# Optimization experiments

Hardware: AMD Instinct MI355X
Metric: run time of the kernel (lower is better)

## Reference

```python
import jax, jax.numpy as jnp
import numpy as np

GROUPS = 8
EPS = 1e-3  # Keras GroupNormalization default epsilon


def group_norm(x, gamma, beta):
    b, h, w, c = x.shape
    xr = x.reshape(b, h, w, GROUPS, c // GROUPS)
    mean = jnp.mean(xr, axis=(1, 2, 4), keepdims=True)
    var = jnp.var(xr, axis=(1, 2, 4), keepdims=True)
    xn = ((xr - mean) * jax.lax.rsqrt(var + EPS)).reshape(b, h, w, c)
    return xn * gamma + beta


def setup_inputs() -> dict:
    key = jax.random.key(0)
    ks = jax.random.split(key, 6)
    B, H, W, C = 4, 64, 64, 256
    std = C ** -0.5
    return {
        "x": jax.random.normal(ks[0], (B, H, W, C), dtype=jnp.float32),
        "gamma": jnp.ones((C,), jnp.float32),
        "beta": jnp.zeros((C,), jnp.float32),
        "wq": jax.random.normal(ks[1], (C, C), jnp.float32) * std,
        "bq": jnp.zeros((C,), jnp.float32),
        "wk": jax.random.normal(ks[2], (C, C), jnp.float32) * std,
        "bk": jnp.zeros((C,), jnp.float32),
        "wv": jax.random.normal(ks[3], (C, C), jnp.float32) * std,
        "bv": jnp.zeros((C,), jnp.float32),
        "wp": jax.random.normal(ks[4], (C, C), jnp.float32) * std,
        "bp": jnp.zeros((C,), jnp.float32),
    }


def reference(x, gamma, beta, wq, bq, wk, bk, wv, bv, wp, bp):
    b, h, w, c = x.shape
    scale = jnp.asarray(c, x.dtype) ** -0.5
    xn = group_norm(x, gamma, beta)
    # 1x1 convs are per-pixel dense layers
    q = (xn @ wq + bq).reshape(b, h * w, c)
    k = (xn @ wk + bk).reshape(b, h * w, c)
    v = (xn @ wv + bv).reshape(b, h * w, c)
    scores = jnp.einsum('bic,bjc->bij', q, k) * scale  # [b, N, N]
    attn = jax.nn.softmax(scores, axis=-1)
    out = jnp.einsum('bij,bjc->bic', attn, v).reshape(b, h, w, c)
    return x + (out @ wp + bp)
```

## Files before the change

kernel.cpp:

```cpp
#include <hip/hip_runtime.h>

#define N_TOK 4096
#define C_DIM 256
#define BATCH 4
#define M_ROWS (BATCH * N_TOK)
#define GN_CNT 131072.0f
#define JSPLIT 4

typedef __attribute__((ext_vector_type(4))) float f32x4;
typedef __attribute__((ext_vector_type(16))) float f32x16;
typedef __attribute__((ext_vector_type(8))) short s16x8;
typedef __attribute__((ext_vector_type(4))) unsigned short u16x4;
typedef __attribute__((ext_vector_type(4))) unsigned int u32x4;

static __device__ __forceinline__ unsigned short f2bf(float f) {
  unsigned int u = __builtin_bit_cast(unsigned int, f);
  u += 0x7fff + ((u >> 16) & 1);
  return (unsigned short)(u >> 16);
}
static __device__ __forceinline__ float bf2f(unsigned short h) {
  unsigned int u = ((unsigned int)h) << 16;
  return __builtin_bit_cast(float, u);
}

static __device__ __forceinline__ void gload_lds16(const void* g, void* l) {
  __builtin_amdgcn_global_load_lds(
      (__attribute__((address_space(1))) void*)(unsigned long long)(const char*)g,
      (__attribute__((address_space(3))) void*)l, 16, 0, 0);
}

__global__ __launch_bounds__(256) void prep(const float* __restrict__ x,
                                            const float* __restrict__ wq,
                                            const float* __restrict__ wk,
                                            const float* __restrict__ wv,
                                            const float* __restrict__ wp,
                                            float* __restrict__ partials,
                                            unsigned short* __restrict__ wT) {
  int tid = threadIdx.x;
  if (blockIdx.x < 512) {
    int bg = blockIdx.x >> 4, chunk = blockIdx.x & 15;
    int b = bg >> 3, g = bg & 7;
    const f32x4* x4 = (const f32x4*)x;
    float s1 = 0.f, s2 = 0.f;
#pragma unroll
    for (int it = 0; it < 8; ++it) {
      int idx = it * 256 + tid;
      int nl = idx >> 3, cq = idx & 7;
      f32x4 v = x4[(b * N_TOK + chunk * 256 + nl) * 64 + g * 8 + cq];
      s1 += v[0] + v[1] + v[2] + v[3];
      s2 += v[0] * v[0] + v[1] * v[1] + v[2] * v[2] + v[3] * v[3];
    }
    for (int m = 1; m < 64; m <<= 1) {
      s1 += __shfl_xor(s1, m, 64);
      s2 += __shfl_xor(s2, m, 64);
    }
    __shared__ float r1[4], r2[4];
    int wave = tid >> 6, lane = tid & 63;
    if (lane == 0) { r1[wave] = s1; r2[wave] = s2; }
    __syncthreads();
    if (tid == 0) {
      int slot = (bg * 16 + chunk) * 2;
      partials[slot]     = r1[0] + r1[1] + r1[2] + r1[3];
      partials[slot + 1] = r2[0] + r2[1] + r2[2] + r2[3];
    }
  } else {
    int rem = blockIdx.x - 512;
    int z = rem >> 6, t = rem & 63;
    int k0 = (t >> 3) * 32, n0 = (t & 7) * 32;
    const float* const srcs[4] = {wq, wk, wv, wp};
    const float* w = srcs[z];
    unsigned short* o = wT + z * 65536;
    __shared__ float tt[32][33];
    int tx = tid & 31, ty = tid >> 5;
#pragma unroll
    for (int ky = 0; ky < 32; ky += 8)
      tt[ty + ky][tx] = w[(k0 + ty + ky) * C_DIM + n0 + tx];
    __syncthreads();
#pragma unroll
    for (int ky = 0; ky < 32; ky += 8)
      o[(n0 + ty + ky) * C_DIM + k0 + tx] = f2bf(tt[tx][ty + ky]);
  }
}

__global__ __launch_bounds__(256, 2) void qkv_gemm(const float* __restrict__ x,
                                                   const unsigned short* __restrict__ wT,
                                                   const float* __restrict__ partials,
                                                   const float* __restrict__ gamma,
                                                   const float* __restrict__ beta,
                                                   const float* __restrict__ bq,
                                                   const float* __restrict__ bk,
                                                   const float* __restrict__ bv,
                                                   unsigned short* __restrict__ qo,
                                                   unsigned short* __restrict__ ko,
                                                   unsigned short* __restrict__ vo) {
  int tid = threadIdx.x;
  int wave = tid >> 6, lane = tid & 63, n32 = lane & 31, half = lane >> 5;
  int row0 = blockIdx.x * 128 + wave * 32;
  int c0 = blockIdx.y * 128;
  int row = row0 + n32;
  int batch = blockIdx.x >> 5;
  __shared__ __align__(16) unsigned short Wt[32768];
  __shared__ float mean_s[8], rstd_s[8];

#pragma unroll
  for (int ii = 0; ii < 32; ++ii) {
    int u = ii * 256 + tid;
    int n = u >> 5, ku = u & 31;
    gload_lds16(wT + (size_t)(c0 + n) * C_DIM + ((ku ^ (n & 7)) * 8), Wt + u * 8);
  }
  if (tid < 8) {
    const float* p = partials + (batch * 8 + tid) * 32;
    float s1 = 0.f, s2 = 0.f;
#pragma unroll
    for (int c = 0; c < 16; ++c) { s1 += p[2 * c]; s2 += p[2 * c + 1]; }
    float inv = 1.f / GN_CNT;
    float m = s1 * inv, v = s2 * inv - m * m;
    mean_s[tid] = m;
    rstd_s[tid] = rsqrtf(v + 1e-3f);
  }
  __syncthreads();

  float mean[8], rstd[8];
#pragma unroll
  for (int g = 0; g < 8; ++g) { mean[g] = mean_s[g]; rstd[g] = rstd_s[g]; }
  s16x8 af[16];
#pragma unroll
  for (int ks = 0; ks < 16; ++ks) {
    int cb = ks * 16 + half * 8;
    const f32x4* xp = (const f32x4*)(x + (size_t)row * C_DIM + cb);
    f32x4 v0 = xp[0], v1 = xp[1];
    const f32x4* g4 = (const f32x4*)(gamma + cb);
    const f32x4* b4 = (const f32x4*)(beta + cb);
    f32x4 ga0 = g4[0], ga1 = g4[1], be0 = b4[0], be1 = b4[1];
    int g = (2 * ks + half) >> 2;
    float m = mean[g], rs = rstd[g];
    s16x8 o;
#pragma unroll
    for (int j = 0; j < 4; ++j) {
      o[j]     = (short)f2bf((v0[j] - m) * rs * ga0[j] + be0[j]);
      o[4 + j] = (short)f2bf((v1[j] - m) * rs * ga1[j] + be1[j]);
    }
    af[ks] = o;
  }

  for (int w = 0; w < 3; ++w) {
    if (w > 0) {
      __syncthreads();
#pragma unroll
      for (int ii = 0; ii < 32; ++ii) {
        int u = ii * 256 + tid;
        int n = u >> 5, ku = u & 31;
        gload_lds16(wT + (size_t)w * 65536 + (size_t)(c0 + n) * C_DIM + ((ku ^ (n & 7)) * 8),
                    Wt + u * 8);
      }
      __syncthreads();
    }
    const float* bias = (w == 0) ? bq : (w == 1) ? bk : bv;
    unsigned short* outp = (w == 0) ? qo : (w == 1) ? ko : vo;
    float scale = (w == 0) ? 0.0625f : 1.f;
#pragma unroll
    for (int ct = 0; ct < 4; ++ct) {
      int nl = ct * 32 + n32;
      f32x16 acc = (f32x16)(bias[c0 + nl]);
#pragma unroll
      for (int ks = 0; ks < 16; ++ks) {
        s16x8 wf = *(const s16x8*)(Wt + nl * C_DIM + (((2 * ks + half) ^ (nl & 7)) * 8));
        acc = __builtin_amdgcn_mfma_f32_32x32x16_bf16(af[ks], wf, acc, 0, 0, 0);
      }
#pragma unroll
      for (int r = 0; r < 16; ++r) {
        int rr = (r & 3) + 8 * (r >> 2) + 4 * half;
        outp[(size_t)(row0 + rr) * C_DIM + c0 + nl] = f2bf(acc[r] * scale);
      }
    }
  }
}

__global__ __launch_bounds__(256) void vtrans(const unsigned short* __restrict__ v,
                                              unsigned short* __restrict__ vT) {
  __shared__ unsigned short t[32][33];
  int n0 = blockIdx.x * 32, c0 = blockIdx.y * 32, b = blockIdx.z;
  int tx = threadIdx.x, ty = threadIdx.y;
#pragma unroll
  for (int ky = 0; ky < 32; ky += 8)
    t[ty + ky][tx] = v[(b * N_TOK + n0 + ty + ky) * C_DIM + c0 + tx];
  __syncthreads();
#pragma unroll
  for (int ky = 0; ky < 32; ky += 8)
    vT[(b * C_DIM + c0 + ty + ky) * N_TOK + n0 + tx] = t[tx][ty + ky];
}

static __device__ __forceinline__ void stage_K(unsigned short* dst,
                                               const unsigned short* kb,
                                               int jbase, int tid) {
#pragma unroll
  for (int ii = 0; ii < 4; ++ii) {
    int u = ii * 256 + tid;
    int ksu = u >> 6, tok = (u >> 1) & 31, hf = u & 1;
    gload_lds16(kb + (size_t)(jbase + tok) * C_DIM + ksu * 16 + hf * 8, dst + u * 8);
  }
}
static __device__ __forceinline__ void stage_V(unsigned short* dst,
                                               const unsigned short* vb,
                                               int jbase, int tid) {
#pragma unroll
  for (int ii = 0; ii < 4; ++ii)
    gload_lds16(vb + (size_t)tid * N_TOK + jbase + ii * 8, dst + (ii * 256 + tid) * 8);
}

static __device__ __forceinline__ f32x16 qk_compute(const unsigned short* KT,
                                                    const s16x8* qf,
                                                    int n32, int half) {
  f32x16 sc = (f32x16)(0.f);
#pragma unroll
  for (int ks = 0; ks < 16; ++ks) {
    s16x8 kf = *(const s16x8*)(KT + ks * 512 + (n32 * 2 + half) * 8);
    sc = __builtin_amdgcn_mfma_f32_32x32x16_bf16(kf, qf[ks], sc, 0, 0, 0);
  }
  return sc;
}

__global__ __launch_bounds__(256, 2) void attn_part(const unsigned short* __restrict__ q,
                                                    const unsigned short* __restrict__ k,
                                                    const unsigned short* __restrict__ vT,
                                                    unsigned short* __restrict__ op0,
                                                    unsigned short* __restrict__ op1,
                                                    unsigned short* __restrict__ op2,
                                                    unsigned short* __restrict__ op3,
                                                    float* __restrict__ lbuf) {
  int tid = threadIdx.x;
  int wave = tid >> 6, lane = tid & 63;
  int n32 = lane & 31, half = lane >> 5;
  int i = blockIdx.x;
  int batch = (i >> 1) & 3;
  int slot = ((i >> 3) << 1) | (i & 1);
  int qb = slot & 31, chunk = slot >> 5;
  int qrow0 = batch * N_TOK + qb * 128 + wave * 32;
  const unsigned short* kb = k + (size_t)batch * N_TOK * C_DIM;
  const unsigned short* vb = vT + (size_t)batch * C_DIM * N_TOK;
  unsigned short* op = (chunk == 0) ? op0 : (chunk == 1) ? op1 : (chunk == 2) ? op2 : op3;

  __shared__ __align__(16) unsigned short K_lds[2][8192];
  __shared__ __align__(16) unsigned short V_lds[3][8192];

  int jbase0 = chunk * 1024;
  stage_K(K_lds[0], kb, jbase0, tid);
  stage_V(V_lds[0], vb, jbase0, tid);

  const unsigned short* qp = q + (size_t)(qrow0 + n32) * C_DIM;
  s16x8 qf[16];
#pragma unroll
  for (int ks = 0; ks < 16; ++ks)
    qf[ks] = *(const s16x8*)(qp + ks * 16 + half * 8);

  f32x16 Oa[8];
#pragma unroll
  for (int ct = 0; ct < 8; ++ct) Oa[ct] = (f32x16)(0.f);
  float ls = 0.f;

  __syncthreads();

  stage_K(K_lds[1], kb, jbase0 + 32, tid);
  stage_V(V_lds[1], vb, jbase0 + 32, tid);

  s16x8 pf0p, pf1p;
  {
    f32x16 sc = qk_compute(K_lds[0], qf, n32, half);
    unsigned D[8], E[8];
#pragma unroll
    for (int t = 0; t < 8; ++t) {
      float pa = exp2f(fmaf(sc[2 * t],     1.44269504f, -11.54156032f));
      float pb = exp2f(fmaf(sc[2 * t + 1], 1.44269504f, -11.54156032f));
      ls += pa + pb;
      D[t] = (__builtin_bit_cast(unsigned, pa) >> 16) |
             (__builtin_bit_cast(unsigned, pb) & 0xFFFF0000u);
      E[t] = __shfl_xor(D[t], 32);
    }
    u32x4 w0 = {half ? E[2] : D[0], half ? E[3] : D[1],
                half ? D[2] : E[0], half ? D[3] : E[1]};
    u32x4 w1 = {half ? E[6] : D[4], half ? E[7] : D[5],
                half ? D[6] : E[4], half ? D[7] : E[5]};
    pf0p = __builtin_bit_cast(s16x8, w0);
    pf1p = __builtin_bit_cast(s16x8, w1);
  }

  int vr_i = 0, vw_i = 2;
  for (int jt = 1; jt < 32; ++jt) {
    __syncthreads();
    if (jt < 31) {
      int jb2 = jbase0 + (jt + 1) * 32;
      stage_K(K_lds[(jt + 1) & 1], kb, jb2, tid);
      stage_V(V_lds[vw_i], vb, jb2, tid);
    }
    __builtin_amdgcn_s_setprio(1);
    f32x16 sc = qk_compute(K_lds[jt & 1], qf, n32, half);

    const unsigned short* VR = V_lds[vr_i];
    unsigned D[8], E[8];
#pragma unroll
    for (int t = 0; t < 8; ++t) {
      float pa = exp2f(fmaf(sc[2 * t],     1.44269504f, -11.54156032f));
      float pb = exp2f(fmaf(sc[2 * t + 1], 1.44269504f, -11.54156032f));
      ls += pa + pb;
      D[t] = (__builtin_bit_cast(unsigned, pa) >> 16) |
             (__builtin_bit_cast(unsigned, pb) & 0xFFFF0000u);
      E[t] = __shfl_xor(D[t], 32);
      int ch = t * 32 + n32;
      s16x8 vf0 = *(const s16x8*)(VR + (half * 256 + ch) * 8);
      s16x8 vf1 = *(const s16x8*)(VR + ((2 + half) * 256 + ch) * 8);
      Oa[t] = __builtin_amdgcn_mfma_f32_32x32x16_bf16(pf0p, vf0, Oa[t], 0, 0, 0);
      Oa[t] = __builtin_amdgcn_mfma_f32_32x32x16_bf16(pf1p, vf1, Oa[t], 0, 0, 0);
    }
    __builtin_amdgcn_s_setprio(0);

    u32x4 w0 = {half ? E[2] : D[0], half ? E[3] : D[1],
                half ? D[2] : E[0], half ? D[3] : E[1]};
    u32x4 w1 = {half ? E[6] : D[4], half ? E[7] : D[5],
                half ? D[6] : E[4], half ? D[7] : E[5]};
    pf0p = __builtin_bit_cast(s16x8, w0);
    pf1p = __builtin_bit_cast(s16x8, w1);
    vr_i = (vr_i == 2) ? 0 : vr_i + 1;
    vw_i = (vw_i == 2) ? 0 : vw_i + 1;
  }

  {
    const unsigned short* VR = V_lds[vr_i];
#pragma unroll
    for (int t = 0; t < 8; ++t) {
      int ch = t * 32 + n32;
      s16x8 vf0 = *(const s16x8*)(VR + (half * 256 + ch) * 8);
      s16x8 vf1 = *(const s16x8*)(VR + ((2 + half) * 256 + ch) * 8);
      Oa[t] = __builtin_amdgcn_mfma_f32_32x32x16_bf16(pf0p, vf0, Oa[t], 0, 0, 0);
      Oa[t] = __builtin_amdgcn_mfma_f32_32x32x16_bf16(pf1p, vf1, Oa[t], 0, 0, 0);
    }
  }

#pragma unroll
  for (int ct = 0; ct < 8; ++ct)
#pragma unroll
    for (int r = 0; r < 16; ++r) {
      int row = (r & 3) + 8 * (r >> 2) + 4 * half;
      op[(size_t)(qrow0 + row) * C_DIM + ct * 32 + n32] = f2bf(Oa[ct][r]);
    }
  float tot = ls + __shfl_xor(ls, 32);
  if (half == 0) lbuf[chunk * M_ROWS + qrow0 + n32] = tot;
}

__global__ __launch_bounds__(256, 2) void proj_gemm(const unsigned short* __restrict__ p0,
                                                    const unsigned short* __restrict__ p1,
                                                    const unsigned short* __restrict__ p2,
                                                    const unsigned short* __restrict__ p3,
                                                    const float* __restrict__ lbuf,
                                                    const unsigned short* __restrict__ wt,
                                                    const float* __restrict__ bp,
                                                    const float* __restrict__ x,
                                                    float* __restrict__ out) {
  int tid = threadIdx.x;
  int wave = tid >> 6, lane = tid & 63, n32 = lane & 31, half = lane >> 5;
  int row0 = blockIdx.x * 128 + wave * 32;
  int c0 = blockIdx.y * 128;
  __shared__ __align__(16) unsigned short Wt[32768];

#pragma unroll
  for (int ii = 0; ii < 32; ++ii) {
    int u = ii * 256 + tid;
    int n = u >> 5, ku = u & 31;
    gload_lds16(wt + (size_t)(c0 + n) * C_DIM + ((ku ^ (n & 7)) * 8), Wt + u * 8);
  }

  int row = row0 + n32;
  float linv = 1.f / (lbuf[row] + lbuf[M_ROWS + row] +
                      lbuf[2 * M_ROWS + row] + lbuf[3 * M_ROWS + row]);
  s16x8 af[16];
#pragma unroll
  for (int ks = 0; ks < 16; ++ks) {
    size_t off = (size_t)row * C_DIM + ks * 16 + half * 8;
    s16x8 a0 = *(const s16x8*)(p0 + off);
    s16x8 a1 = *(const s16x8*)(p1 + off);
    s16x8 a2 = *(const s16x8*)(p2 + off);
    s16x8 a3 = *(const s16x8*)(p3 + off);
    s16x8 o;
#pragma unroll
    for (int j = 0; j < 8; ++j) {
      float f = bf2f((unsigned short)a0[j]) + bf2f((unsigned short)a1[j]) +
                bf2f((unsigned short)a2[j]) + bf2f((unsigned short)a3[j]);
      o[j] = (short)f2bf(f * linv);
    }
    af[ks] = o;
  }
  __syncthreads();

#pragma unroll
  for (int ct = 0; ct < 4; ++ct) {
    int nl = ct * 32 + n32;
    f32x16 acc = (f32x16)(bp[c0 + nl]);
#pragma unroll
    for (int ks = 0; ks < 16; ++ks) {
      s16x8 wf = *(const s16x8*)(Wt + nl * C_DIM + (((2 * ks + half) ^ (nl & 7)) * 8));
      acc = __builtin_amdgcn_mfma_f32_32x32x16_bf16(af[ks], wf, acc, 0, 0, 0);
    }
#pragma unroll
    for (int r = 0; r < 16; ++r) {
      int rr = (r & 3) + 8 * (r >> 2) + 4 * half;
      size_t idx = (size_t)(row0 + rr) * C_DIM + c0 + nl;
      out[idx] = acc[r] + x[idx];
    }
  }
}

extern "C" void kernel_launch(void* const* d_in, const int* in_sizes, int n_in,
                              void* d_out, int out_size, void* d_ws, size_t ws_size,
                              hipStream_t stream) {
  const float* x     = (const float*)d_in[0];
  const float* gamma = (const float*)d_in[1];
  const float* beta  = (const float*)d_in[2];
  const float* wq    = (const float*)d_in[3];
  const float* bq    = (const float*)d_in[4];
  const float* wk    = (const float*)d_in[5];
  const float* bk    = (const float*)d_in[6];
  const float* wv    = (const float*)d_in[7];
  const float* bv    = (const float*)d_in[8];
  const float* wp    = (const float*)d_in[9];
  const float* bp    = (const float*)d_in[10];
  float* out = (float*)d_out;

  char* ws = (char*)d_ws;
  const size_t MC = (size_t)M_ROWS * C_DIM;
  float* partials      = (float*)ws;
  unsigned short* wT   = (unsigned short*)(ws + 4096);
  unsigned short* qb   = wT + 4 * 65536;
  unsigned short* kbuf = qb + MC;
  unsigned short* vb   = kbuf + MC;
  unsigned short* vTb  = vb + MC;
  unsigned short* pl0  = vTb + MC;
  unsigned short* pl2  = pl0 + MC;
  unsigned short* pl3  = pl2 + MC;
  float* lbuf          = (float*)(pl3 + MC);
  unsigned short* pl1  = vb;

  prep<<<768, 256, 0, stream>>>(x, wq, wk, wv, wp, partials, wT);
  qkv_gemm<<<dim3(128, 2), 256, 0, stream>>>(x, wT, partials, gamma, beta,
                                             bq, bk, bv, qb, kbuf, vb);
  vtrans<<<dim3(128, 8, 4), dim3(32, 8), 0, stream>>>(vb, vTb);
  attn_part<<<512, 256, 0, stream>>>(qb, kbuf, vTb, pl0, pl1, pl2, pl3, lbuf);
  proj_gemm<<<dim3(128, 2), 256, 0, stream>>>(pl0, pl1, pl2, pl3, lbuf,
                                              wT + 3 * 65536, bp, x, out);
}
```

Before: 222.3 us.

## Split attention waves into QK producers and channel-half PV consumers via LDS

```diff
diff --git a/kernel.cpp b/kernel.cpp
--- a/kernel.cpp
+++ b/kernel.cpp
@@ -5,7 +5,6 @@
 #define BATCH 4
 #define M_ROWS (BATCH * N_TOK)
 #define GN_CNT 131072.0f
-#define JSPLIT 4
 
 typedef __attribute__((ext_vector_type(4))) float f32x4;
 typedef __attribute__((ext_vector_type(16))) float f32x16;
@@ -220,7 +219,7 @@
   return sc;
 }
 
-__global__ __launch_bounds__(256, 2) void attn_part(const unsigned short* __restrict__ q,
+__global__ __launch_bounds__(256, 3) void attn_part(const unsigned short* __restrict__ q,
                                                     const unsigned short* __restrict__ k,
                                                     const unsigned short* __restrict__ vT,
                                                     unsigned short* __restrict__ op0,
@@ -231,119 +230,98 @@
   int tid = threadIdx.x;
   int wave = tid >> 6, lane = tid & 63;
   int n32 = lane & 31, half = lane >> 5;
-  int i = blockIdx.x;
-  int batch = (i >> 1) & 3;
-  int slot = ((i >> 3) << 1) | (i & 1);
-  int qb = slot & 31, chunk = slot >> 5;
-  int qrow0 = batch * N_TOK + qb * 128 + wave * 32;
+  int rg = wave >> 1, chv = wave & 1;
+  int bid = blockIdx.x;
+  int chunk = bid >> 8;
+  int rowslot = bid & 255;
+  int batch = rowslot >> 6, qslot = rowslot & 63;
+  int qrow0 = batch * N_TOK + qslot * 64 + rg * 32;
   const unsigned short* kb = k + (size_t)batch * N_TOK * C_DIM;
   const unsigned short* vb = vT + (size_t)batch * C_DIM * N_TOK;
   unsigned short* op = (chunk == 0) ? op0 : (chunk == 1) ? op1 : (chunk == 2) ? op2 : op3;
 
-  __shared__ __align__(16) unsigned short K_lds[2][8192];
-  __shared__ __align__(16) unsigned short V_lds[3][8192];
+  __shared__ __align__(16) unsigned short K_lds[8192];
+  __shared__ __align__(16) unsigned short V_lds[2][8192];
+  __shared__ __align__(16) unsigned short P_lds[2][2][512];
 
   int jbase0 = chunk * 1024;
-  stage_K(K_lds[0], kb, jbase0, tid);
+  stage_K(K_lds, kb, jbase0, tid);
   stage_V(V_lds[0], vb, jbase0, tid);
 
-  const unsigned short* qp = q + (size_t)(qrow0 + n32) * C_DIM;
   s16x8 qf[16];
-#pragma unroll
-  for (int ks = 0; ks < 16; ++ks)
-    qf[ks] = *(const s16x8*)(qp + ks * 16 + half * 8);
-
-  f32x16 Oa[8];
-#pragma unroll
-  for (int ct = 0; ct < 8; ++ct) Oa[ct] = (f32x16)(0.f);
+  if (chv == 0) {
+    const unsigned short* qp = q + (size_t)(qrow0 + n32) * C_DIM;
+#pragma unroll
+    for (int ks = 0; ks < 16; ++ks)
+      qf[ks] = *(const s16x8*)(qp + ks * 16 + half * 8);
+  }
+
+  f32x16 Oa[4];
+#pragma unroll
+  for (int t = 0; t < 4; ++t) Oa[t] = (f32x16)(0.f);
   float ls = 0.f;
 
-  __syncthreads();
-
-  stage_K(K_lds[1], kb, jbase0 + 32, tid);
-  stage_V(V_lds[1], vb, jbase0 + 32, tid);
-
-  s16x8 pf0p, pf1p;
-  {
-    f32x16 sc = qk_compute(K_lds[0], qf, n32, half);
-    unsigned D[8], E[8];
-#pragma unroll
-    for (int t = 0; t < 8; ++t) {
-      float pa = exp2f(fmaf(sc[2 * t],     1.44269504f, -11.54156032f));
-      float pb = exp2f(fmaf(sc[2 * t + 1], 1.44269504f, -11.54156032f));
-      ls += pa + pb;
-      D[t] = (__builtin_bit_cast(unsigned, pa) >> 16) |
-             (__builtin_bit_cast(unsigned, pb) & 0xFFFF0000u);
-      E[t] = __shfl_xor(D[t], 32);
-    }
-    u32x4 w0 = {half ? E[2] : D[0], half ? E[3] : D[1],
-                half ? D[2] : E[0], half ? D[3] : E[1]};
-    u32x4 w1 = {half ? E[6] : D[4], half ? E[7] : D[5],
-                half ? D[6] : E[4], half ? D[7] : E[5]};
-    pf0p = __builtin_bit_cast(s16x8, w0);
-    pf1p = __builtin_bit_cast(s16x8, w1);
-  }
-
-  int vr_i = 0, vw_i = 2;
-  for (int jt = 1; jt < 32; ++jt) {
-    __syncthreads();
-    if (jt < 31) {
-      int jb2 = jbase0 + (jt + 1) * 32;
-      stage_K(K_lds[(jt + 1) & 1], kb, jb2, tid);
-      stage_V(V_lds[vw_i], vb, jb2, tid);
-    }
+  for (int jt = 0; jt < 32; ++jt) {
+    asm volatile("s_waitcnt vmcnt(0)" ::: "memory");
+    __builtin_amdgcn_s_barrier();
+    __builtin_amdgcn_sched_barrier(0);
+    if (jt < 31)
+      stage_V(V_lds[(jt + 1) & 1], vb, jbase0 + (jt + 1) * 32, tid);
+    if (chv == 0) {
+      __builtin_amdgcn_s_setprio(1);
+      f32x16 sc = qk_compute(K_lds, qf, n32, half);
+      __builtin_amdgcn_s_setprio(0);
+      unsigned D[8];
+#pragma unroll
+      for (int t = 0; t < 8; ++t) {
+        float pa = exp2f(fmaf(sc[2 * t],     1.44269504f, -11.54156032f));
+        float pb = exp2f(fmaf(sc[2 * t + 1], 1.44269504f, -11.54156032f));
+        ls += pa + pb;
+        D[t] = (__builtin_bit_cast(unsigned, pa) >> 16) |
+               (__builtin_bit_cast(unsigned, pb) & 0xFFFF0000u);
+      }
+      unsigned E[8];
+#pragma unroll
+      for (int t = 0; t < 8; ++t) E[t] = __shfl_xor(D[t], 32);
+      u32x4 w0 = {half ? E[2] : D[0], half ? E[3] : D[1],
+                  half ? D[2] : E[0], half ? D[3] : E[1]};
+      u32x4 w1 = {half ? E[6] : D[4], half ? E[7] : D[5],
+                  half ? D[6] : E[4], half ? D[7] : E[1 + 4]};
+      w1[3] = half ? D[7] : E[5];
+      *(u32x4*)(&P_lds[rg][0][lane * 8]) = w0;
+      *(u32x4*)(&P_lds[rg][1][lane * 8]) = w1;
+    }
+    asm volatile("s_waitcnt lgkmcnt(0)" ::: "memory");
+    __builtin_amdgcn_s_barrier();
+    __builtin_amdgcn_sched_barrier(0);
+    if (jt < 31)
+      stage_K(K_lds, kb, jbase0 + (jt + 1) * 32, tid);
+    s16x8 pf0 = *(const s16x8*)(&P_lds[rg][0][lane * 8]);
+    s16x8 pf1 = *(const s16x8*)(&P_lds[rg][1][lane * 8]);
+    const unsigned short* VR = V_lds[jt & 1];
     __builtin_amdgcn_s_setprio(1);
-    f32x16 sc = qk_compute(K_lds[jt & 1], qf, n32, half);
-
-    const unsigned short* VR = V_lds[vr_i];
-    unsigned D[8], E[8];
-#pragma unroll
-    for (int t = 0; t < 8; ++t) {
-      float pa = exp2f(fmaf(sc[2 * t],     1.44269504f, -11.54156032f));
-      float pb = exp2f(fmaf(sc[2 * t + 1], 1.44269504f, -11.54156032f));
-      ls += pa + pb;
-      D[t] = (__builtin_bit_cast(unsigned, pa) >> 16) |
-             (__builtin_bit_cast(unsigned, pb) & 0xFFFF0000u);
-      E[t] = __shfl_xor(D[t], 32);
-      int ch = t * 32 + n32;
+#pragma unroll
+    for (int t = 0; t < 4; ++t) {
+      int ch = chv * 128 + t * 32 + n32;
       s16x8 vf0 = *(const s16x8*)(VR + (half * 256 + ch) * 8);
       s16x8 vf1 = *(const s16x8*)(VR + ((2 + half) * 256 + ch) * 8);
-      Oa[t] = __builtin_amdgcn_mfma_f32_32x32x16_bf16(pf0p, vf0, Oa[t], 0, 0, 0);
-      Oa[t] = __builtin_amdgcn_mfma_f32_32x32x16_bf16(pf1p, vf1, Oa[t], 0, 0, 0);
+      Oa[t] = __builtin_amdgcn_mfma_f32_32x32x16_bf16(pf0, vf0, Oa[t], 0, 0, 0);
+      Oa[t] = __builtin_amdgcn_mfma_f32_32x32x16_bf16(pf1, vf1, Oa[t], 0, 0, 0);
     }
     __builtin_amdgcn_s_setprio(0);
-
-    u32x4 w0 = {half ? E[2] : D[0], half ? E[3] : D[1],
-                half ? D[2] : E[0], half ? D[3] : E[1]};
-    u32x4 w1 = {half ? E[6] : D[4], half ? E[7] : D[5],
-                half ? D[6] : E[4], half ? D[7] : E[5]};
-    pf0p = __builtin_bit_cast(s16x8, w0);
-    pf1p = __builtin_bit_cast(s16x8, w1);
-    vr_i = (vr_i == 2) ? 0 : vr_i + 1;
-    vw_i = (vw_i == 2) ? 0 : vw_i + 1;
-  }
-
-  {
-    const unsigned short* VR = V_lds[vr_i];
-#pragma unroll
-    for (int t = 0; t < 8; ++t) {
-      int ch = t * 32 + n32;
-      s16x8 vf0 = *(const s16x8*)(VR + (half * 256 + ch) * 8);
-      s16x8 vf1 = *(const s16x8*)(VR + ((2 + half) * 256 + ch) * 8);
-      Oa[t] = __builtin_amdgcn_mfma_f32_32x32x16_bf16(pf0p, vf0, Oa[t], 0, 0, 0);
-      Oa[t] = __builtin_amdgcn_mfma_f32_32x32x16_bf16(pf1p, vf1, Oa[t], 0, 0, 0);
-    }
-  }
-
-#pragma unroll
-  for (int ct = 0; ct < 8; ++ct)
+  }
+
+#pragma unroll
+  for (int ct = 0; ct < 4; ++ct)
 #pragma unroll
     for (int r = 0; r < 16; ++r) {
       int row = (r & 3) + 8 * (r >> 2) + 4 * half;
-      op[(size_t)(qrow0 + row) * C_DIM + ct * 32 + n32] = f2bf(Oa[ct][r]);
-    }
-  float tot = ls + __shfl_xor(ls, 32);
-  if (half == 0) lbuf[chunk * M_ROWS + qrow0 + n32] = tot;
+      op[(size_t)(qrow0 + row) * C_DIM + chv * 128 + ct * 32 + n32] = f2bf(Oa[ct][r]);
+    }
+  if (chv == 0) {
+    float tot = ls + __shfl_xor(ls, 32);
+    if (half == 0) lbuf[chunk * M_ROWS + qrow0 + n32] = tot;
+  }
 }
 
 __global__ __launch_bounds__(256, 2) void proj_gemm(const unsigned short* __restrict__ p0,
@@ -442,7 +420,7 @@
   qkv_gemm<<<dim3(128, 2), 256, 0, stream>>>(x, wT, partials, gamma, beta,
                                              bq, bk, bv, qb, kbuf, vb);
   vtrans<<<dim3(128, 8, 4), dim3(32, 8), 0, stream>>>(vb, vTb);
-  attn_part<<<512, 256, 0, stream>>>(qb, kbuf, vTb, pl0, pl1, pl2, pl3, lbuf);
+  attn_part<<<1024, 256, 0, stream>>>(qb, kbuf, vTb, pl0, pl1, pl2, pl3, lbuf);
   proj_gemm<<<dim3(128, 2), 256, 0, stream>>>(pl0, pl1, pl2, pl3, lbuf,
                                               wT + 3 * 65536, bp, x, out);
 }
```

Measured after the change: 343.4 us. 54.5% more time.
